# Kernel tuning notes

Hardware: AMD Instinct MI355X
Metric: run time of the kernel (lower is better)

## Reference

```python
import jax, jax.numpy as jnp
import numpy as np

B, S, D = 2, 2048, 2048
H, KV, HD = 32, 8, 64          # n_heads, n_kv_heads, head_dim
REP = H // KV                  # 4
THETA = 10000.0


def _rotate_half(u):
    h = u.shape[-1] // 2
    return jnp.concatenate([-u[..., h:], u[..., :h]], axis=-1)


def setup_inputs() -> dict:
    key = jax.random.key(0)
    ks = jax.random.split(key, 5)
    x = jax.random.normal(ks[0], (B, S, D), dtype=jnp.float32)
    Wq = jax.random.normal(ks[1], (D, H * HD), dtype=jnp.float32) * 0.02
    Wk = jax.random.normal(ks[2], (D, KV * HD), dtype=jnp.float32) * 0.02
    Wv = jax.random.normal(ks[3], (D, KV * HD), dtype=jnp.float32) * 0.02
    Wo = jax.random.normal(ks[4], (H * HD, D), dtype=jnp.float32) * 0.02
    return {"x": x, "Wq": Wq, "Wk": Wk, "Wv": Wv, "Wo": Wo}


def reference(x, Wq, Wk, Wv, Wo):
    b, s, d = x.shape
    # QKV projections (nn.Linear, no bias)
    q = (x @ Wq).reshape(b, s, H, HD).transpose(0, 2, 1, 3)   # [B,H,S,HD]
    k = (x @ Wk).reshape(b, s, KV, HD).transpose(0, 2, 1, 3)  # [B,KV,S,HD]
    v = (x @ Wv).reshape(b, s, KV, HD).transpose(0, 2, 1, 3)  # [B,KV,S,HD]

    # RoPE (position_offset = 0)
    inv_freq = 1.0 / (THETA ** (jnp.arange(0, HD, 2, dtype=jnp.float32) / HD))
    freqs = jnp.outer(jnp.arange(s, dtype=jnp.float32), inv_freq)  # [S,HD/2]
    emb = jnp.concatenate([freqs, freqs], axis=-1)                  # [S,HD]
    cos, sin = jnp.cos(emb), jnp.sin(emb)
    q = q * cos + _rotate_half(q) * sin
    k = k * cos + _rotate_half(k) * sin

    # Grouped attention: avoid materializing repeated KV tensors.
    qg = q.reshape(b, KV, REP, s, HD)                               # [B,KV,REP,S,HD]
    scale = 1.0 / np.sqrt(HD)
    scores = jnp.einsum('bgrqd,bgkd->bgrqk', qg, k) * scale         # [B,KV,REP,S,S]
    causal = jnp.tril(jnp.ones((s, s), dtype=bool))
    scores = jnp.where(causal, scores, jnp.finfo(jnp.float32).min)
    probs = jax.nn.softmax(scores.astype(jnp.float32), axis=-1).astype(q.dtype)
    out = jnp.einsum('bgrqk,bgkd->bgrqd', probs, v)                 # [B,KV,REP,S,HD]
    out = out.reshape(b, H, s, HD).transpose(0, 2, 1, 3).reshape(b, s, H * HD)
    return out @ Wo                                                  # [B,S,D]
```

## Files before the change

### kernel.cpp

```cpp
#include <hip/hip_runtime.h>
#include <math.h>

typedef __bf16 bf16_t;
typedef bf16_t bf16x8 __attribute__((ext_vector_type(8)));
typedef bf16_t bf16x4 __attribute__((ext_vector_type(4)));
typedef float floatx4 __attribute__((ext_vector_type(4)));
typedef short short4v __attribute__((ext_vector_type(4)));

#define MFMA16(a, b, c) __builtin_amdgcn_mfma_f32_16x16x32_bf16((a), (b), (c), 0, 0, 0)

#if __has_builtin(__builtin_amdgcn_exp2f)
#define PEXP(x) __builtin_amdgcn_exp2f(x)
#define SCORE_SCALE (0.125f * 1.4426950408889634f)
#else
#define PEXP(x) __expf(x)
#define SCORE_SCALE 0.125f
#endif

#if __has_builtin(__builtin_amdgcn_mfma_f32_16x16x16bf16_1k)
#define HAVE_MFMA_K16 1
__device__ __forceinline__ floatx4 mfma_k16(bf16x4 a, bf16x4 b, floatx4 c)
{
    union { bf16x4 v; short4v s; } ua, ub;
    ua.v = a; ub.v = b;
    return __builtin_amdgcn_mfma_f32_16x16x16bf16_1k(ua.s, ub.s, c, 0, 0, 0);
}
#endif

union PU { unsigned u[2]; bf16x4 v; };
union BU { unsigned u[4]; bf16x8 v; };

__device__ __forceinline__ void gld16(const void* g, void* lds)
{
    __builtin_amdgcn_global_load_lds(
        reinterpret_cast<const __attribute__((address_space(1))) void*>(
            reinterpret_cast<uintptr_t>(g)),
        reinterpret_cast<__attribute__((address_space(3))) void*>(
            (unsigned int)reinterpret_cast<uintptr_t>(lds)),
        16, 0, 0);
}

__device__ __forceinline__ void stage128(
    const bf16_t* __restrict__ g, int K, int r0, int k0,
    bf16_t* lds, int tid, int wave)
{
    #pragma unroll
    for (int i = 0; i < 4; ++i) {
        int c = i * 256 + tid, r = c >> 3, s = c & 7;
        gld16(g + (size_t)(r0 + r) * K + k0 + ((s ^ (r & 7)) << 3),
              lds + (size_t)(i * 256 + wave * 64) * 8);
    }
}

template <typename TC>
__device__ __forceinline__ void gemm128_body(
    const bf16_t* __restrict__ A, const bf16_t* __restrict__ Bt,
    TC* __restrict__ C, int row0, int col0, int N, int K,
    bf16_t* As, bf16_t* Bs)
{
    const int tid  = threadIdx.x;
    const int wave = tid >> 6, lane = tid & 63;
    const int quad = lane >> 4, l16 = lane & 15;
    const int wm = (wave >> 1) * 64;
    const int wn = (wave & 1) * 64;

    const int ntile = K >> 6;

    floatx4 acc[4][4] = {};

    #pragma unroll 1
    for (int u = 0; u < ntile; ++u) {
        __syncthreads();
        stage128(A, K, row0, u << 6, As, tid, wave);
        stage128(Bt, K, col0, u << 6, Bs, tid, wave);
        __syncthreads();

        bf16x8 af[4][2], bfr[4][2];
        #pragma unroll
        for (int mt = 0; mt < 4; ++mt)
            #pragma unroll
            for (int kh = 0; kh < 2; ++kh) {
                int ar = wm + mt * 16 + l16;
                af[mt][kh] = *(const bf16x8*)&As[ar * 64 +
                    (((kh * 4 + quad) ^ (ar & 7)) << 3)];
            }
        #pragma unroll
        for (int nt = 0; nt < 4; ++nt)
            #pragma unroll
            for (int kh = 0; kh < 2; ++kh) {
                int br = wn + nt * 16 + l16;
                bfr[nt][kh] = *(const bf16x8*)&Bs[br * 64 +
                    (((kh * 4 + quad) ^ (br & 7)) << 3)];
            }

        __builtin_amdgcn_s_setprio(1);
        #pragma unroll
        for (int kh = 0; kh < 2; ++kh)
            #pragma unroll
            for (int mt = 0; mt < 4; ++mt)
                #pragma unroll
                for (int nt = 0; nt < 4; ++nt)
                    acc[mt][nt] = MFMA16(af[mt][kh], bfr[nt][kh], acc[mt][nt]);
        __builtin_amdgcn_s_setprio(0);
    }

    #pragma unroll
    for (int mt = 0; mt < 4; ++mt)
        #pragma unroll
        for (int nt = 0; nt < 4; ++nt)
            #pragma unroll
            for (int r = 0; r < 4; ++r)
                C[(size_t)(row0 + wm + mt * 16 + quad * 4 + r) * N
                  + col0 + wn + nt * 16 + l16] = (TC)acc[mt][nt][r];
}

__global__ __launch_bounds__(256, 3) void gemm128_qkv(
    const bf16_t* __restrict__ A, const bf16_t* __restrict__ BtQ,
    const bf16_t* __restrict__ BtK, const bf16_t* __restrict__ BtV,
    bf16_t* __restrict__ CQ, bf16_t* __restrict__ CK, bf16_t* __restrict__ CV)
{
    __shared__ alignas(16) bf16_t As[128 * 64];
    __shared__ alignas(16) bf16_t Bs[128 * 64];
    const int bid = blockIdx.x;
    const int l = (bid & 7) * 96 + (bid >> 3);
    const int x = l % 24;
    const int y = l / 24;
    const bf16_t* Bt; bf16_t* C; int N, col0;
    if (x < 16)      { Bt = BtQ; C = CQ; N = 2048; col0 = x * 128; }
    else if (x < 20) { Bt = BtK; C = CK; N = 512;  col0 = (x - 16) * 128; }
    else             { Bt = BtV; C = CV; N = 512;  col0 = (x - 20) * 128; }
    gemm128_body<bf16_t>(A, Bt, C, y * 128, col0, N, 2048, As, Bs);
}

__global__ __launch_bounds__(256, 3) void gemm128_out(
    const bf16_t* __restrict__ A, const bf16_t* __restrict__ Bt,
    float* __restrict__ C)
{
    __shared__ alignas(16) bf16_t As[128 * 64];
    __shared__ alignas(16) bf16_t Bs[128 * 64];
    const int bid = blockIdx.x;
    const int l = (bid & 7) * 64 + (bid >> 3);
    const int x = l & 15;
    const int y = l >> 4;
    gemm128_body<float>(A, Bt, C, y * 128, x * 128, 2048, 2048, As, Bs);
}

__device__ __forceinline__ void transpose_body(
    const float* __restrict__ W, bf16_t* __restrict__ Wt, int K, int N,
    int bx, int by, float (*t)[33], int tid)
{
    int tx = tid & 31, ty = tid >> 5;
    #pragma unroll
    for (int i = 0; i < 32; i += 8)
        t[ty + i][tx] = W[(size_t)(by + ty + i) * N + bx + tx];
    __syncthreads();
    #pragma unroll
    for (int i = 0; i < 32; i += 8)
        Wt[(size_t)(bx + ty + i) * K + by + tx] = (bf16_t)t[tx][ty + i];
}

__global__ __launch_bounds__(256) void prep_all(
    const float* __restrict__ x, const float* __restrict__ Wq,
    const float* __restrict__ Wk, const float* __restrict__ Wv,
    bf16_t* __restrict__ xb, bf16_t* __restrict__ WqT,
    bf16_t* __restrict__ WkT, bf16_t* __restrict__ WvT)
{
    __shared__ float t[32][33];
    const int blk = blockIdx.x, tid = threadIdx.x;
    if (blk < 8192) {
        int i = blk * 256 + tid;
        float4 f = ((const float4*)x)[i];
        bf16x4 v = {(bf16_t)f.x, (bf16_t)f.y, (bf16_t)f.z, (bf16_t)f.w};
        ((bf16x4*)xb)[i] = v;
    } else if (blk < 12288) {
        int r = blk - 8192;
        transpose_body(Wq, WqT, 2048, 2048, (r & 63) * 32, (r >> 6) * 32, t, tid);
    } else if (blk < 13312) {
        int r = blk - 12288;
        transpose_body(Wk, WkT, 2048, 512, (r & 15) * 32, (r >> 4) * 32, t, tid);
    } else {
        int r = blk - 13312;
        transpose_body(Wv, WvT, 2048, 512, (r & 15) * 32, (r >> 4) * 32, t, tid);
    }
}

__global__ __launch_bounds__(256) void mid_all(
    bf16_t* __restrict__ Kw, const bf16_t* __restrict__ Vw,
    bf16_t* __restrict__ VtG, const float* __restrict__ Wo,
    bf16_t* __restrict__ WoT)
{
    __shared__ float tf[32][33];
    __shared__ bf16_t tb[32][34];
    const int blk = blockIdx.x, tid = threadIdx.x;
    if (blk < 4096) {
        int idx = blk * 256 + tid;
        int i   = idx & 31;
        int h   = (idx >> 5) & 7;
        int row = idx >> 8;
        int pos = row & 2047;
        float invf = powf(10000.0f, -(float)i / 32.0f);
        float sv, cv;
        sincosf((float)pos * invf, &sv, &cv);
        size_t base = (size_t)row * 512 + (size_t)h * 64 + i;
        float a  = (float)Kw[base];
        float b2 = (float)Kw[base + 32];
        Kw[base]      = (bf16_t)(a * cv - b2 * sv);
        Kw[base + 32] = (bf16_t)(b2 * cv + a * sv);
    } else if (blk < 6144) {
        int r  = blk - 4096;
        int bz = r >> 10, r2 = r & 1023;
        int bx = (r2 & 15) * 32, by = (r2 >> 4) * 32;
        int tx = tid & 31, ty = tid >> 5;
        #pragma unroll
        for (int i = 0; i < 32; i += 8)
            tb[ty + i][tx] = Vw[((size_t)bz * 2048 + by + ty + i) * 512 + bx + tx];
        __syncthreads();
        #pragma unroll
        for (int i = 0; i < 32; i += 8)
            VtG[((size_t)bz * 512 + bx + ty + i) * 2048 + by + tx] = tb[tx][ty + i];
    } else {
        int r = blk - 6144;
        transpose_body(Wo, WoT, 2048, 2048, (r & 63) * 32, (r >> 6) * 32, tf, tid);
    }
}

__global__ __launch_bounds__(256, 2) void gqa_attn(
    const bf16_t* __restrict__ Q, const bf16_t* __restrict__ Kc,
    const bf16_t* __restrict__ Vt, bf16_t* __restrict__ AO)
{
    __shared__ alignas(16) bf16_t Ks[2][128 * 64];
    __shared__ alignas(16) bf16_t Vs[2][128 * 64];

    const int bid = blockIdx.x;
    const int l   = (bid & 7) * 64 + (bid >> 3);
    const int g   = l >> 6;
    const int b   = (l >> 5) & 1;
    const int x   = l & 31;

    const int tid  = threadIdx.x;
    const int wave = tid >> 6, lane = tid & 63;
    const int quad = lane >> 4, l16 = lane & 15;
    const int h = g * 4 + wave;

    #pragma unroll 1
    for (int t = 0; t < 2; ++t) {
        const int qt = t ? x : (63 - x);
        const int q0 = qt * 32;
        int qb[2];
        qb[0] = q0;
        qb[1] = q0 + 16;

        bf16x8 qf[2][2];
        #pragma unroll
        for (int mt = 0; mt < 2; ++mt) {
            int qrow = qb[mt] + l16;
            const bf16_t* qp = Q + (size_t)(b * 2048 + qrow) * 2048 + h * 64 + quad * 8;
            bf16x8 lo = *(const bf16x8*)qp;
            bf16x8 hi = *(const bf16x8*)(qp + 32);
            #pragma unroll
            for (int j = 0; j < 8; ++j) {
                int d = quad * 8 + j;
                float invf = powf(10000.0f, -(float)d / 32.0f);
                float sv, cv;
                sincosf((float)qrow * invf, &sv, &cv);
                float a = (float)lo[j], c2 = (float)hi[j];
                qf[mt][0][j] = (bf16_t)((a * cv - c2 * sv) * SCORE_SCALE);
                qf[mt][1][j] = (bf16_t)((c2 * cv + a * sv) * SCORE_SCALE);
            }
        }

        floatx4 o[2][4] = {};
        floatx4 ls4[2] = {};

        const int ktmax = qt >> 1;
        const int nwin  = (ktmax >> 1) + 1;

        auto STAGE = [&](int win, int dst) {
            const int kbase = win * 128;
            #pragma unroll
            for (int i = 0; i < 4; ++i) {
                int c = i * 256 + tid, r = c >> 3, s = c & 7;
                int sw = (s ^ (r & 7)) << 3;
                gld16(Kc + (size_t)(b * 2048 + kbase + r) * 512 + g * 64 + sw,
                      &Ks[dst][(i * 256 + wave * 64) * 8]);
            }
            #pragma unroll
            for (int i = 0; i < 4; ++i) {
                int c = i * 256 + tid;
                int ci = c & 511, hw = c >> 9;
                int r = ci >> 3, s = ci & 7;
                int sw = (s ^ (r & 7)) << 3;
                gld16(Vt + (size_t)(b * 512 + g * 64 + r) * 2048
                         + kbase + hw * 64 + sw,
                      &Vs[dst][(i * 256 + wave * 64) * 8]);
            }
        };

        __asm__ volatile("s_waitcnt lgkmcnt(0)" ::: "memory");
        __builtin_amdgcn_s_barrier();
        STAGE(0, 0);

        #pragma unroll 1
        for (int win = 0; win < nwin; ++win) {
            const int cur = win & 1;
            if (win + 1 < nwin) {
                STAGE(win + 1, cur ^ 1);
                __asm__ volatile("s_waitcnt vmcnt(8)" ::: "memory");
            } else {
                __asm__ volatile("s_waitcnt vmcnt(0)" ::: "memory");
            }
            __builtin_amdgcn_s_barrier();

            #pragma unroll
            for (int hw = 0; hw < 2; ++hw) {
                const int kt = 2 * win + hw;
                if (kt <= ktmax) {
                    const bf16_t* Ksh = &Ks[cur][hw * 4096];
                    const bf16_t* Vsh = &Vs[cur][hw * 4096];

                    floatx4 st[2][4] = {};
                    __builtin_amdgcn_s_setprio(1);
                    #pragma unroll
                    for (int nt = 0; nt < 4; ++nt) {
                        int kr = nt * 16 + l16;
                        bf16x8 kf0 = *(const bf16x8*)&Ksh[kr * 64 + ((quad ^ (kr & 7)) << 3)];
                        bf16x8 kf1 = *(const bf16x8*)&Ksh[kr * 64 + (((4 + quad) ^ (kr & 7)) << 3)];
                        st[0][nt] = MFMA16(kf0, qf[0][0], st[0][nt]);
                        st[0][nt] = MFMA16(kf1, qf[0][1], st[0][nt]);
                        st[1][nt] = MFMA16(kf0, qf[1][0], st[1][nt]);
                        st[1][nt] = MFMA16(kf1, qf[1][1], st[1][nt]);
                    }
                    __builtin_amdgcn_s_setprio(0);

                    PU pk[2][4];
                    const bool diag = (kt == ktmax);
                    #pragma unroll
                    for (int mt = 0; mt < 2; ++mt) {
                        const int qa = qb[mt] + l16;
                        #pragma unroll
                        for (int nt = 0; nt < 4; ++nt) {
                            float pv[4];
                            #pragma unroll
                            for (int r = 0; r < 4; ++r) {
                                float e = PEXP(st[mt][nt][r]);
                                if (diag) {
                                    int ka = kt * 64 + nt * 16 + quad * 4 + r;
                                    if (ka > qa) e = 0.f;
                                }
                                ls4[mt][r] += e;
                                pv[r] = e;
                            }
                            pk[mt][nt].v = bf16x4{(bf16_t)pv[0], (bf16_t)pv[1],
                                                  (bf16_t)pv[2], (bf16_t)pv[3]};
                        }
                    }

#ifdef HAVE_MFMA_K16
                    __builtin_amdgcn_s_setprio(1);
                    #pragma unroll
                    for (int nt = 0; nt < 4; ++nt)
                        #pragma unroll
                        for (int dt = 0; dt < 4; ++dt) {
                            int vr = dt * 16 + l16;
                            int slot = ((nt << 1) | (quad >> 1)) ^ (vr & 7);
                            bf16x4 va = *(const bf16x4*)&Vsh[vr * 64 + (slot << 3)
                                                             + ((quad & 1) << 2)];
                            o[0][dt] = mfma_k16(va, pk[0][nt].v, o[0][dt]);
                            o[1][dt] = mfma_k16(va, pk[1][nt].v, o[1][dt]);
                        }
                    __builtin_amdgcn_s_setprio(0);
#else
                    #pragma unroll
                    for (int H = 0; H < 2; ++H) {
                        BU bfv[2];
                        #pragma unroll
                        for (int mt = 0; mt < 2; ++mt) {
                            #pragma unroll
                            for (int j = 0; j < 4; ++j) {
                                int srcl = (((quad & 1) << 1) + (j >> 1)) * 16 + l16;
                                unsigned a0 = (unsigned)__shfl((int)pk[mt][2 * H].u[j & 1], srcl, 64);
                                unsigned a1 = (unsigned)__shfl((int)pk[mt][2 * H + 1].u[j & 1], srcl, 64);
                                bfv[mt].u[j] = (quad >> 1) ? a1 : a0;
                            }
                        }
                        #pragma unroll
                        for (int dt = 0; dt < 4; ++dt) {
                            int vr = dt * 16 + l16;
                            bf16x8 va = *(const bf16x8*)&Vsh[vr * 64
                                          + ((((H << 2) | quad) ^ (vr & 7)) << 3)];
                            o[0][dt] = MFMA16(va, bfv[0].v, o[0][dt]);
                            o[1][dt] = MFMA16(va, bfv[1].v, o[1][dt]);
                        }
                    }
#endif
                }
            }

            __asm__ volatile("s_waitcnt lgkmcnt(0)" ::: "memory");
            __builtin_amdgcn_s_barrier();
        }

        #pragma unroll
        for (int mt = 0; mt < 2; ++mt) {
            float l2 = ls4[mt][0] + ls4[mt][1] + ls4[mt][2] + ls4[mt][3];
            l2 += __shfl_xor(l2, 16, 64);
            l2 += __shfl_xor(l2, 32, 64);
            float rc = 1.0f / l2;
            #pragma unroll
            for (int dt = 0; dt < 4; ++dt) {
                bf16x4 ov = {(bf16_t)(o[mt][dt][0] * rc), (bf16_t)(o[mt][dt][1] * rc),
                             (bf16_t)(o[mt][dt][2] * rc), (bf16_t)(o[mt][dt][3] * rc)};
                *(bf16x4*)&AO[(size_t)(b * 2048 + qb[mt] + l16) * 2048
                              + h * 64 + dt * 16 + quad * 4] = ov;
            }
        }
    }
}

extern "C" void kernel_launch(void* const* d_in, const int* in_sizes, int n_in,
                              void* d_out, int out_size, void* d_ws, size_t ws_size,
                              hipStream_t stream)
{
    const float* x  = (const float*)d_in[0];
    const float* Wq = (const float*)d_in[1];
    const float* Wk = (const float*)d_in[2];
    const float* Wv = (const float*)d_in[3];
    const float* Wo = (const float*)d_in[4];
    float* out = (float*)d_out;

    const size_t MB = 1024 * 1024;
    char* ws = (char*)d_ws;
    bf16_t* xb_AO = (bf16_t*)(ws);
    bf16_t* WqoT  = (bf16_t*)(ws + 16 * MB);
    bf16_t* WkT   = (bf16_t*)(ws + 24 * MB);
    bf16_t* WvT   = (bf16_t*)(ws + 26 * MB);
    bf16_t* Qw    = (bf16_t*)(ws + 28 * MB);
    bf16_t* Kw    = (bf16_t*)(ws + 44 * MB);
    bf16_t* Vw    = (bf16_t*)(ws + 48 * MB);
    bf16_t* VtG   = (bf16_t*)(ws + 52 * MB);

    prep_all<<<14336, 256, 0, stream>>>(x, Wq, Wk, Wv, xb_AO, WqoT, WkT, WvT);

    gemm128_qkv<<<dim3(768), 256, 0, stream>>>(
        xb_AO, WqoT, WkT, WvT, Qw, Kw, Vw);

    mid_all<<<10240, 256, 0, stream>>>(Kw, Vw, VtG, Wo, WqoT);

    gqa_attn<<<dim3(512), 256, 0, stream>>>(Qw, Kw, VtG, xb_AO);

    gemm128_out<<<dim3(512), 256, 0, stream>>>(xb_AO, WqoT, out);
}
```

Before: 275.1 us.

## Shrink attention tiles to 16 query rows and 64-key windows for occupancy

The attention kernel now gives each wave one 16-row query tile instead of two and stages 64-key K/V windows instead of 128. LDS use halves, launch bounds rise to four blocks per CU, and the grid doubles to 1024 blocks. The aim is more parallelism and latency hiding on the many CUs of the GPU. In exchange, each K/V fragment loaded from LDS feeds half as many MFMAs, so there is more global and LDS traffic per unit of compute and more barriers per key.

```diff
diff --git a/kernel.cpp b/kernel.cpp
--- a/kernel.cpp
+++ b/kernel.cpp
@@ -224,18 +224,18 @@
     }
 }
 
-__global__ __launch_bounds__(256, 2) void gqa_attn(
+__global__ __launch_bounds__(256, 4) void gqa_attn(
     const bf16_t* __restrict__ Q, const bf16_t* __restrict__ Kc,
     const bf16_t* __restrict__ Vt, bf16_t* __restrict__ AO)
 {
-    __shared__ alignas(16) bf16_t Ks[2][128 * 64];
-    __shared__ alignas(16) bf16_t Vs[2][128 * 64];
+    __shared__ alignas(16) bf16_t Ks[2][64 * 64];
+    __shared__ alignas(16) bf16_t Vs[2][64 * 64];
 
     const int bid = blockIdx.x;
-    const int l   = (bid & 7) * 64 + (bid >> 3);
-    const int g   = l >> 6;
-    const int b   = (l >> 5) & 1;
-    const int x   = l & 31;
+    const int l   = (bid & 7) * 128 + (bid >> 3);
+    const int g   = l >> 7;
+    const int b   = (l >> 6) & 1;
+    const int x   = l & 63;
 
     const int tid  = threadIdx.x;
     const int wave = tid >> 6, lane = tid & 63;
@@ -244,16 +244,12 @@
 
     #pragma unroll 1
     for (int t = 0; t < 2; ++t) {
-        const int qt = t ? x : (63 - x);
-        const int q0 = qt * 32;
-        int qb[2];
-        qb[0] = q0;
-        qb[1] = q0 + 16;
-
-        bf16x8 qf[2][2];
-        #pragma unroll
-        for (int mt = 0; mt < 2; ++mt) {
-            int qrow = qb[mt] + l16;
+        const int qt = t ? x : (127 - x);
+        const int qb = qt * 16;
+
+        bf16x8 qf[2];
+        {
+            int qrow = qb + l16;
             const bf16_t* qp = Q + (size_t)(b * 2048 + qrow) * 2048 + h * 64 + quad * 8;
             bf16x8 lo = *(const bf16x8*)qp;
             bf16x8 hi = *(const bf16x8*)(qp + 32);
@@ -264,155 +260,131 @@
                 float sv, cv;
                 sincosf((float)qrow * invf, &sv, &cv);
                 float a = (float)lo[j], c2 = (float)hi[j];
-                qf[mt][0][j] = (bf16_t)((a * cv - c2 * sv) * SCORE_SCALE);
-                qf[mt][1][j] = (bf16_t)((c2 * cv + a * sv) * SCORE_SCALE);
+                qf[0][j] = (bf16_t)((a * cv - c2 * sv) * SCORE_SCALE);
+                qf[1][j] = (bf16_t)((c2 * cv + a * sv) * SCORE_SCALE);
             }
         }
 
-        floatx4 o[2][4] = {};
-        floatx4 ls4[2] = {};
-
-        const int ktmax = qt >> 1;
-        const int nwin  = (ktmax >> 1) + 1;
-
-        auto STAGE = [&](int win, int dst) {
-            const int kbase = win * 128;
-            #pragma unroll
-            for (int i = 0; i < 4; ++i) {
-                int c = i * 256 + tid, r = c >> 3, s = c & 7;
-                int sw = (s ^ (r & 7)) << 3;
-                gld16(Kc + (size_t)(b * 2048 + kbase + r) * 512 + g * 64 + sw,
-                      &Ks[dst][(i * 256 + wave * 64) * 8]);
-            }
-            #pragma unroll
-            for (int i = 0; i < 4; ++i) {
-                int c = i * 256 + tid;
-                int ci = c & 511, hw = c >> 9;
-                int r = ci >> 3, s = ci & 7;
-                int sw = (s ^ (r & 7)) << 3;
-                gld16(Vt + (size_t)(b * 512 + g * 64 + r) * 2048
-                         + kbase + hw * 64 + sw,
-                      &Vs[dst][(i * 256 + wave * 64) * 8]);
-            }
-        };
+        floatx4 o[4] = {};
+        floatx4 ls4 = {};
+
+        const int ktmax = qt >> 2;
 
         __asm__ volatile("s_waitcnt lgkmcnt(0)" ::: "memory");
         __builtin_amdgcn_s_barrier();
-        STAGE(0, 0);
+        #pragma unroll
+        for (int i = 0; i < 2; ++i) {
+            int c = i * 256 + tid;
+            int r = c >> 3, s = c & 7;
+            int sw = (s ^ (r & 7)) << 3;
+            gld16(Kc + (size_t)(b * 2048 + r) * 512 + g * 64 + sw,
+                  &Ks[0][(i * 256 + wave * 64) * 8]);
+            gld16(Vt + (size_t)(b * 512 + g * 64 + r) * 2048 + sw,
+                  &Vs[0][(i * 256 + wave * 64) * 8]);
+        }
 
         #pragma unroll 1
-        for (int win = 0; win < nwin; ++win) {
-            const int cur = win & 1;
-            if (win + 1 < nwin) {
-                STAGE(win + 1, cur ^ 1);
-                __asm__ volatile("s_waitcnt vmcnt(8)" ::: "memory");
+        for (int kt = 0; kt <= ktmax; ++kt) {
+            const int cur = kt & 1;
+            if (kt < ktmax) {
+                const int kn = kt + 1;
+                #pragma unroll
+                for (int i = 0; i < 2; ++i) {
+                    int c = i * 256 + tid;
+                    int r = c >> 3, s = c & 7;
+                    int sw = (s ^ (r & 7)) << 3;
+                    gld16(Kc + (size_t)(b * 2048 + kn * 64 + r) * 512 + g * 64 + sw,
+                          &Ks[cur ^ 1][(i * 256 + wave * 64) * 8]);
+                    gld16(Vt + (size_t)(b * 512 + g * 64 + r) * 2048 + kn * 64 + sw,
+                          &Vs[cur ^ 1][(i * 256 + wave * 64) * 8]);
+                }
+                __asm__ volatile("s_waitcnt vmcnt(4)" ::: "memory");
             } else {
                 __asm__ volatile("s_waitcnt vmcnt(0)" ::: "memory");
             }
             __builtin_amdgcn_s_barrier();
 
-            #pragma unroll
-            for (int hw = 0; hw < 2; ++hw) {
-                const int kt = 2 * win + hw;
-                if (kt <= ktmax) {
-                    const bf16_t* Ksh = &Ks[cur][hw * 4096];
-                    const bf16_t* Vsh = &Vs[cur][hw * 4096];
-
-                    floatx4 st[2][4] = {};
-                    __builtin_amdgcn_s_setprio(1);
+            floatx4 st[4] = {};
+            __builtin_amdgcn_s_setprio(1);
+            #pragma unroll
+            for (int nt = 0; nt < 4; ++nt) {
+                int kr = nt * 16 + l16;
+                bf16x8 kf0 = *(const bf16x8*)&Ks[cur][kr * 64 + ((quad ^ (kr & 7)) << 3)];
+                bf16x8 kf1 = *(const bf16x8*)&Ks[cur][kr * 64 + (((4 + quad) ^ (kr & 7)) << 3)];
+                st[nt] = MFMA16(kf0, qf[0], st[nt]);
+                st[nt] = MFMA16(kf1, qf[1], st[nt]);
+            }
+            __builtin_amdgcn_s_setprio(0);
+
+            PU pk[4];
+            {
+                const bool diag = (kt == ktmax);
+                const int qa = qb + l16;
+                #pragma unroll
+                for (int nt = 0; nt < 4; ++nt) {
+                    float pv[4];
                     #pragma unroll
-                    for (int nt = 0; nt < 4; ++nt) {
-                        int kr = nt * 16 + l16;
-                        bf16x8 kf0 = *(const bf16x8*)&Ksh[kr * 64 + ((quad ^ (kr & 7)) << 3)];
-                        bf16x8 kf1 = *(const bf16x8*)&Ksh[kr * 64 + (((4 + quad) ^ (kr & 7)) << 3)];
-                        st[0][nt] = MFMA16(kf0, qf[0][0], st[0][nt]);
-                        st[0][nt] = MFMA16(kf1, qf[0][1], st[0][nt]);
-                        st[1][nt] = MFMA16(kf0, qf[1][0], st[1][nt]);
-                        st[1][nt] = MFMA16(kf1, qf[1][1], st[1][nt]);
+                    for (int r = 0; r < 4; ++r) {
+                        float e = PEXP(st[nt][r]);
+                        if (diag) {
+                            int ka = kt * 64 + nt * 16 + quad * 4 + r;
+                            if (ka > qa) e = 0.f;
+                        }
+                        ls4[r] += e;
+                        pv[r] = e;
                     }
-                    __builtin_amdgcn_s_setprio(0);
-
-                    PU pk[2][4];
-                    const bool diag = (kt == ktmax);
-                    #pragma unroll
-                    for (int mt = 0; mt < 2; ++mt) {
-                        const int qa = qb[mt] + l16;
-                        #pragma unroll
-                        for (int nt = 0; nt < 4; ++nt) {
-                            float pv[4];
-                            #pragma unroll
-                            for (int r = 0; r < 4; ++r) {
-                                float e = PEXP(st[mt][nt][r]);
-                                if (diag) {
-                                    int ka = kt * 64 + nt * 16 + quad * 4 + r;
-                                    if (ka > qa) e = 0.f;
-                                }
-                                ls4[mt][r] += e;
-                                pv[r] = e;
-                            }
-                            pk[mt][nt].v = bf16x4{(bf16_t)pv[0], (bf16_t)pv[1],
-                                                  (bf16_t)pv[2], (bf16_t)pv[3]};
-                        }
-                    }
+                    pk[nt].v = bf16x4{(bf16_t)pv[0], (bf16_t)pv[1],
+                                      (bf16_t)pv[2], (bf16_t)pv[3]};
+                }
+            }
 
 #ifdef HAVE_MFMA_K16
-                    __builtin_amdgcn_s_setprio(1);
-                    #pragma unroll
-                    for (int nt = 0; nt < 4; ++nt)
-                        #pragma unroll
-                        for (int dt = 0; dt < 4; ++dt) {
-                            int vr = dt * 16 + l16;
-                            int slot = ((nt << 1) | (quad >> 1)) ^ (vr & 7);
-                            bf16x4 va = *(const bf16x4*)&Vsh[vr * 64 + (slot << 3)
-                                                             + ((quad & 1) << 2)];
-                            o[0][dt] = mfma_k16(va, pk[0][nt].v, o[0][dt]);
-                            o[1][dt] = mfma_k16(va, pk[1][nt].v, o[1][dt]);
-                        }
-                    __builtin_amdgcn_s_setprio(0);
+            __builtin_amdgcn_s_setprio(1);
+            #pragma unroll
+            for (int nt = 0; nt < 4; ++nt)
+                #pragma unroll
+                for (int dt = 0; dt < 4; ++dt) {
+                    int vr = dt * 16 + l16;
+                    int slot = ((nt << 1) | (quad >> 1)) ^ (vr & 7);
+                    bf16x4 va = *(const bf16x4*)&Vs[cur][vr * 64 + (slot << 3)
+                                                         + ((quad & 1) << 2)];
+                    o[dt] = mfma_k16(va, pk[nt].v, o[dt]);
+                }
+            __builtin_amdgcn_s_setprio(0);
 #else
-                    #pragma unroll
-                    for (int H = 0; H < 2; ++H) {
-                        BU bfv[2];
-                        #pragma unroll
-                        for (int mt = 0; mt < 2; ++mt) {
-                            #pragma unroll
-                            for (int j = 0; j < 4; ++j) {
-                                int srcl = (((quad & 1) << 1) + (j >> 1)) * 16 + l16;
-                                unsigned a0 = (unsigned)__shfl((int)pk[mt][2 * H].u[j & 1], srcl, 64);
-                                unsigned a1 = (unsigned)__shfl((int)pk[mt][2 * H + 1].u[j & 1], srcl, 64);
-                                bfv[mt].u[j] = (quad >> 1) ? a1 : a0;
-                            }
-                        }
-                        #pragma unroll
-                        for (int dt = 0; dt < 4; ++dt) {
-                            int vr = dt * 16 + l16;
-                            bf16x8 va = *(const bf16x8*)&Vsh[vr * 64
-                                          + ((((H << 2) | quad) ^ (vr & 7)) << 3)];
-                            o[0][dt] = MFMA16(va, bfv[0].v, o[0][dt]);
-                            o[1][dt] = MFMA16(va, bfv[1].v, o[1][dt]);
-                        }
-                    }
+            #pragma unroll
+            for (int H = 0; H < 2; ++H) {
+                BU bfv;
+                #pragma unroll
+                for (int j = 0; j < 4; ++j) {
+                    int srcl = (((quad & 1) << 1) + (j >> 1)) * 16 + l16;
+                    unsigned a0 = (unsigned)__shfl((int)pk[2 * H].u[j & 1], srcl, 64);
+                    unsigned a1 = (unsigned)__shfl((int)pk[2 * H + 1].u[j & 1], srcl, 64);
+                    bfv.u[j] = (quad >> 1) ? a1 : a0;
+                }
+                #pragma unroll
+                for (int dt = 0; dt < 4; ++dt) {
+                    int vr = dt * 16 + l16;
+                    bf16x8 va = *(const bf16x8*)&Vs[cur][vr * 64
+                                  + ((((H << 2) | quad) ^ (vr & 7)) << 3)];
+                    o[dt] = MFMA16(va, bfv.v, o[dt]);
+                }
+            }
 #endif
-                }
-            }
-
             __asm__ volatile("s_waitcnt lgkmcnt(0)" ::: "memory");
             __builtin_amdgcn_s_barrier();
         }
 
-        #pragma unroll
-        for (int mt = 0; mt < 2; ++mt) {
-            float l2 = ls4[mt][0] + ls4[mt][1] + ls4[mt][2] + ls4[mt][3];
-            l2 += __shfl_xor(l2, 16, 64);
-            l2 += __shfl_xor(l2, 32, 64);
-            float rc = 1.0f / l2;
-            #pragma unroll
-            for (int dt = 0; dt < 4; ++dt) {
-                bf16x4 ov = {(bf16_t)(o[mt][dt][0] * rc), (bf16_t)(o[mt][dt][1] * rc),
-                             (bf16_t)(o[mt][dt][2] * rc), (bf16_t)(o[mt][dt][3] * rc)};
-                *(bf16x4*)&AO[(size_t)(b * 2048 + qb[mt] + l16) * 2048
-                              + h * 64 + dt * 16 + quad * 4] = ov;
-            }
+        float l2 = ls4[0] + ls4[1] + ls4[2] + ls4[3];
+        l2 += __shfl_xor(l2, 16, 64);
+        l2 += __shfl_xor(l2, 32, 64);
+        float rc = 1.0f / l2;
+        #pragma unroll
+        for (int dt = 0; dt < 4; ++dt) {
+            bf16x4 ov = {(bf16_t)(o[dt][0] * rc), (bf16_t)(o[dt][1] * rc),
+                         (bf16_t)(o[dt][2] * rc), (bf16_t)(o[dt][3] * rc)};
+            *(bf16x4*)&AO[(size_t)(b * 2048 + qb + l16) * 2048
+                          + h * 64 + dt * 16 + quad * 4] = ov;
         }
     }
 }
@@ -446,7 +418,7 @@
 
     mid_all<<<10240, 256, 0, stream>>>(Kw, Vw, VtG, Wo, WqoT);
 
-    gqa_attn<<<dim3(512), 256, 0, stream>>>(Qw, Kw, VtG, xb_AO);
+    gqa_attn<<<dim3(1024), 256, 0, stream>>>(Qw, Kw, VtG, xb_AO);
 
     gemm128_out<<<dim3(512), 256, 0, stream>>>(xb_AO, WqoT, out);
 }
```

Measured after the change: 279.7 us. Within noise of the previous version (+1.7%).
